# Kernel tuning notes

Measured on AMD Instinct MI355X. Metric: run time of the kernel, lower is better.

Reference implementation:

```python
import jax, jax.numpy as jnp
import numpy as np

T_STEPS = 60   # args.T
DT = 0.5       # args.dt

def rho(x):
    # repo's rho: hard-sigmoid clamp to [0, 1]
    return jnp.clip(x, 0.0, 1.0)

def setup_inputs() -> dict:
    key = jax.random.key(0)
    k1, k2, k3, k4 = jax.random.split(key, 4)
    B, n0, n1, n_in = 256, 512, 2048, 4096  # size_tab = [n0, n1, n_in]
    data = jax.random.uniform(k1, (B, n_in), dtype=jnp.float32)
    s0 = jnp.zeros((B, n0), jnp.float32)  # initHidden -> zeros
    s1 = jnp.zeros((B, n1), jnp.float32)
    # Linear-style init scales
    w0 = jax.random.normal(k2, (n0, n1), jnp.float32) / np.sqrt(n1)   # Linear(n1->n0), bias
    b0 = jnp.zeros((n0,), jnp.float32)
    w1 = jnp.transpose(w0)                                            # backward weights = w0^T (angle=0)
    w2 = jax.random.normal(k4, (n1, n_in), jnp.float32) / np.sqrt(n_in)  # Linear(n_in->n1), bias
    b2 = jnp.zeros((n1,), jnp.float32)
    return {"data": data, "s0": s0, "s1": s1, "w0": w0, "b0": b0, "w1": w1, "w2": w2, "b2": b2}

def reference(data, s0, s1, w0, b0, w1, w2, b2):
    # forward(method='nograd', beta=0): T forward-Euler stepper iterations, clamped states.
    rd = rho(data)
    inp1 = rd @ w2.T + b2  # data drive is constant over time; hoist out of the scan

    def step(carry, _):
        s0, s1 = carry
        ds0 = -s0 + rho(s1) @ w0.T + b0
        ds1 = -s1 + inp1 + rho(s0) @ w1.T
        s0 = jnp.clip(s0 + DT * ds0, 0.0, 1.0)
        s1 = jnp.clip(s1 + DT * ds1, 0.0, 1.0)
        return (s0, s1), None

    (s0, s1), _ = jax.lax.scan(step, (s0, s1), None, length=T_STEPS)
    return (s0, s1)
```

## Files before the change

### kernel.cpp

```cpp
#include <hip/hip_runtime.h>

typedef unsigned short u16;
typedef __attribute__((ext_vector_type(8))) short short8;
typedef __attribute__((ext_vector_type(4))) float f32x4;

#define BATCH 256
#define N0    512
#define N1    2048
#define NIN   4096
#define TSTEPS 60

static __device__ __forceinline__ f32x4 MFMA(short8 a, short8 b, f32x4 c) {
    return __builtin_amdgcn_mfma_f32_16x16x32_bf16(a, b, c, 0, 0, 0);
}

static __device__ __forceinline__ void split1(float x, u16* __restrict__ hp, u16* __restrict__ lp) {
    unsigned bx = __float_as_uint(x);
    *hp = (u16)(bx >> 16);
    float lf = x - __uint_as_float(bx & 0xFFFF0000u);
    *lp = (u16)(__float_as_uint(lf) >> 16);
}

static __device__ __forceinline__ float clamp01(float v) {
    return fminf(fmaxf(v, 0.0f), 1.0f);
}

static __device__ __forceinline__ size_t apos(int row, int col, int KT) {
    return ((size_t)((row >> 4) * KT + (col >> 5)) * 64
            + (size_t)((row & 15) | (((col >> 3) & 3) << 4))) * 8 + (col & 7);
}

__global__ __launch_bounds__(256) void prep_kernel(
    const float* __restrict__ w0, const float* __restrict__ w1,
    const float* __restrict__ w2, const float* __restrict__ data,
    const float* __restrict__ s0, const float* __restrict__ s1,
    u16* __restrict__ w0h, u16* __restrict__ w0l,
    u16* __restrict__ w1h, u16* __restrict__ w1l,
    u16* __restrict__ w2h, u16* __restrict__ w2l,
    u16* __restrict__ dh,  u16* __restrict__ dl,
    float* __restrict__ s0f, float* __restrict__ s1f,
    u16* __restrict__ s0h, u16* __restrict__ s0l,
    u16* __restrict__ s1h, u16* __restrict__ s1l)
{
    const int tid = blockIdx.x * 256 + threadIdx.x;
    const int nth = gridDim.x * 256;
    u16 h, l;
    for (int i = tid; i < N0 * N1; i += nth) {
        split1(w0[i], &h, &l);
        size_t p = apos(i >> 11, i & 2047, 64);
        w0h[p] = h; w0l[p] = l;
        split1(w1[i], &h, &l);
        p = apos(i >> 9, i & 511, 16);
        w1h[p] = h; w1l[p] = l;
        split1(data[i], &h, &l);
        p = apos(i >> 12, i & 4095, 128);
        dh[p] = h; dl[p] = l;
    }
    for (int i = tid; i < N1 * NIN; i += nth) {
        split1(w2[i], &h, &l);
        size_t p = apos(i >> 12, i & 4095, 128);
        w2h[p] = h; w2l[p] = l;
    }
    for (int i = tid; i < BATCH * N0; i += nth) {
        float v = s0[i]; s0f[i] = v;
        split1(v, &h, &l);
        size_t p = apos(i >> 9, i & 511, 16);
        s0h[p] = h; s0l[p] = l;
    }
    for (int i = tid; i < BATCH * N1; i += nth) {
        float v = s1[i]; s1f[i] = v;
        split1(v, &h, &l);
        size_t p = apos(i >> 11, i & 2047, 64);
        s1h[p] = h; s1l[p] = l;
    }
}

__global__ __launch_bounds__(256) void inp1_kernel(
    const u16* __restrict__ dh, const u16* __restrict__ dl,
    const u16* __restrict__ w2h, const u16* __restrict__ w2l,
    float* __restrict__ partial)
{
    const int wave = threadIdx.x >> 6, lane = threadIdx.x & 63;
    const int lrow = lane & 15, lr4 = (lane >> 4) << 2;
    const int wid = (int)blockIdx.x * 4 + wave;
    const int chunk = wid >> 11, t = wid & 2047;
    const int mt = t >> 7, nt = t & 127;
    const int kt0 = chunk * 32;

    const u16* pah = dh  + ((size_t)(mt * 128 + kt0) * 64 + lane) * 8;
    const u16* pal = dl  + ((size_t)(mt * 128 + kt0) * 64 + lane) * 8;
    const u16* pbh = w2h + ((size_t)(nt * 128 + kt0) * 64 + lane) * 8;
    const u16* pbl = w2l + ((size_t)(nt * 128 + kt0) * 64 + lane) * 8;

    f32x4 acc0 = {}, acc1 = {}, acc2 = {};
    #pragma unroll 4
    for (int i = 0; i < 32; ++i) {
        short8 ah = *(const short8*)(pah + i * 512);
        short8 al = *(const short8*)(pal + i * 512);
        short8 bh = *(const short8*)(pbh + i * 512);
        short8 bl = *(const short8*)(pbl + i * 512);
        acc0 = MFMA(ah, bh, acc0);
        acc1 = MFMA(ah, bl, acc1);
        acc2 = MFMA(al, bh, acc2);
    }
    float* out = partial + (size_t)chunk * BATCH * N1;
    const int col = nt * 16 + lrow;
    #pragma unroll
    for (int r = 0; r < 4; ++r) {
        const int row = mt * 16 + lr4 + r;
        out[(size_t)row * N1 + col] = acc0[r] + acc1[r] + acc2[r];
    }
}

__global__ __launch_bounds__(256) void reduce_kernel(
    const float* __restrict__ partial, const float* __restrict__ b2,
    float* __restrict__ inp1)
{
    const int e = blockIdx.x * 256 + threadIdx.x;
    const float4* p0 = (const float4*)partial;
    const float4* p1 = p0 + (BATCH * N1 / 4);
    const float4* p2 = p1 + (BATCH * N1 / 4);
    const float4* p3 = p2 + (BATCH * N1 / 4);
    const float4 b = ((const float4*)b2)[e & (N1 / 4 - 1)];
    float4 a0 = p0[e], a1 = p1[e], a2 = p2[e], a3 = p3[e];
    float4 r;
    r.x = a0.x + a1.x + a2.x + a3.x + b.x;
    r.y = a0.y + a1.y + a2.y + a3.y + b.y;
    r.z = a0.z + a1.z + a2.z + a3.z + b.z;
    r.w = a0.w + a1.w + a2.w + a3.w + b.w;
    ((float4*)inp1)[e] = r;
}

__global__ __launch_bounds__(256, 6) void step_kernel(
    const float* __restrict__ s0f_in, const float* __restrict__ s1f_in,
    const u16* __restrict__ s0h, const u16* __restrict__ s0l,
    const u16* __restrict__ s1h, const u16* __restrict__ s1l,
    const u16* __restrict__ w0h, const u16* __restrict__ w0l,
    const u16* __restrict__ w1h, const u16* __restrict__ w1l,
    const float* __restrict__ inp1, const float* __restrict__ b0,
    float* __restrict__ s0f_out, float* __restrict__ s1f_out,
    u16* __restrict__ s0h_out, u16* __restrict__ s0l_out,
    u16* __restrict__ s1h_out, u16* __restrict__ s1l_out)
{
    __shared__ float red[4][16][32];
    const int wg = blockIdx.x;
    const int wave = threadIdx.x >> 6, lane = threadIdx.x & 63;
    const int lrow = lane & 15, lr4 = (lane >> 4) << 2;
    const int tid = (int)threadIdx.x;

    if (wg < 1024) {
        const int mt = wg >> 6, ng = wg & 63;
        const int nfrag = wave & 1, kh = wave >> 1;
        const int nt = ng * 2 + nfrag;
        const u16* pah = s0h + ((size_t)(mt * 16 + kh * 8) * 64 + lane) * 8;
        const u16* pal = s0l + ((size_t)(mt * 16 + kh * 8) * 64 + lane) * 8;
        const u16* pbh = w1h + ((size_t)(nt * 16 + kh * 8) * 64 + lane) * 8;
        const u16* pbl = w1l + ((size_t)(nt * 16 + kh * 8) * 64 + lane) * 8;
        f32x4 acc0 = {}, acc1 = {}, acc2 = {};
        #pragma unroll 4
        for (int i = 0; i < 8; ++i) {
            short8 ah = *(const short8*)(pah + i * 512);
            short8 al = *(const short8*)(pal + i * 512);
            short8 bh = *(const short8*)(pbh + i * 512);
            short8 bl = *(const short8*)(pbl + i * 512);
            acc0 = MFMA(ah, bh, acc0);
            acc1 = MFMA(ah, bl, acc1);
            acc2 = MFMA(al, bh, acc2);
        }
        #pragma unroll
        for (int r = 0; r < 4; ++r)
            red[kh][lr4 + r][nfrag * 16 + lrow] = acc0[r] + acc1[r] + acc2[r];
        __syncthreads();
        const int mbase = mt * 16, nbase = ng * 32;
        #pragma unroll
        for (int e = tid; e < 512; e += 256) {
            const int r_ = e >> 5, c_ = e & 31;
            const int row = mbase + r_, col = nbase + c_;
            const float sum = red[0][r_][c_] + red[1][r_][c_];
            const size_t idx = (size_t)row * N1 + col;
            float v = 0.5f * (s1f_in[idx] + inp1[idx] + sum);
            v = clamp01(v);
            s1f_out[idx] = v;
            u16 h, l; split1(v, &h, &l);
            const size_t p = apos(row, col, 64);
            s1h_out[p] = h; s1l_out[p] = l;
        }
    } else {
        const int local = wg - 1024;
        const int rt = local >> 5, ct = local & 31;
        const u16* pah = s1h + ((size_t)(rt * 64 + wave * 16) * 64 + lane) * 8;
        const u16* pal = s1l + ((size_t)(rt * 64 + wave * 16) * 64 + lane) * 8;
        const u16* pbh = w0h + ((size_t)(ct * 64 + wave * 16) * 64 + lane) * 8;
        const u16* pbl = w0l + ((size_t)(ct * 64 + wave * 16) * 64 + lane) * 8;
        f32x4 acc0 = {}, acc1 = {}, acc2 = {};
        #pragma unroll 4
        for (int i = 0; i < 16; ++i) {
            short8 ah = *(const short8*)(pah + i * 512);
            short8 al = *(const short8*)(pal + i * 512);
            short8 bh = *(const short8*)(pbh + i * 512);
            short8 bl = *(const short8*)(pbl + i * 512);
            acc0 = MFMA(ah, bh, acc0);
            acc1 = MFMA(ah, bl, acc1);
            acc2 = MFMA(al, bh, acc2);
        }
        #pragma unroll
        for (int r = 0; r < 4; ++r)
            red[wave][lr4 + r][lrow] = acc0[r] + acc1[r] + acc2[r];
        __syncthreads();
        {
            const int r_ = tid >> 4, c_ = tid & 15;
            const int row = rt * 16 + r_, col = ct * 16 + c_;
            const float sum = red[0][r_][c_] + red[1][r_][c_]
                            + red[2][r_][c_] + red[3][r_][c_];
            const size_t idx = (size_t)row * N0 + col;
            float v = 0.5f * (s0f_in[idx] + sum + b0[col]);
            v = clamp01(v);
            s0f_out[idx] = v;
            u16 h, l; split1(v, &h, &l);
            const size_t p = apos(row, col, 16);
            s0h_out[p] = h; s0l_out[p] = l;
        }
    }
}

extern "C" void kernel_launch(void* const* d_in, const int* in_sizes, int n_in,
                              void* d_out, int out_size, void* d_ws, size_t ws_size,
                              hipStream_t stream) {
    const float* data = (const float*)d_in[0];
    const float* s0_0 = (const float*)d_in[1];
    const float* s1_0 = (const float*)d_in[2];
    const float* w0   = (const float*)d_in[3];
    const float* b0   = (const float*)d_in[4];
    const float* w1   = (const float*)d_in[5];
    const float* w2   = (const float*)d_in[6];
    const float* b2   = (const float*)d_in[7];

    char* p = (char*)d_ws;
    auto alloc = [&](size_t bytes) -> char* {
        char* r = p;
        p += (bytes + 255) & ~(size_t)255;
        return r;
    };
    u16* w0h = (u16*)alloc(N0 * N1 * sizeof(u16));
    u16* w0l = (u16*)alloc(N0 * N1 * sizeof(u16));
    u16* w1h = (u16*)alloc(N0 * N1 * sizeof(u16));
    u16* w1l = (u16*)alloc(N0 * N1 * sizeof(u16));
    u16* w2h = (u16*)alloc((size_t)N1 * NIN * sizeof(u16));
    u16* w2l = (u16*)alloc((size_t)N1 * NIN * sizeof(u16));
    u16* dh  = (u16*)alloc((size_t)BATCH * NIN * sizeof(u16));
    u16* dl  = (u16*)alloc((size_t)BATCH * NIN * sizeof(u16));
    float* partial = (float*)alloc((size_t)4 * BATCH * N1 * sizeof(float));
    float* inp1 = (float*)alloc((size_t)BATCH * N1 * sizeof(float));
    float* s0f[2], *s1f[2];
    u16 *s0h[2], *s0l[2], *s1h[2], *s1l[2];
    for (int i = 0; i < 2; ++i) {
        s0f[i] = (float*)alloc((size_t)BATCH * N0 * sizeof(float));
        s1f[i] = (float*)alloc((size_t)BATCH * N1 * sizeof(float));
        s0h[i] = (u16*)alloc((size_t)BATCH * N0 * sizeof(u16));
        s0l[i] = (u16*)alloc((size_t)BATCH * N0 * sizeof(u16));
        s1h[i] = (u16*)alloc((size_t)BATCH * N1 * sizeof(u16));
        s1l[i] = (u16*)alloc((size_t)BATCH * N1 * sizeof(u16));
    }

    prep_kernel<<<2048, 256, 0, stream>>>(w0, w1, w2, data, s0_0, s1_0,
                                          w0h, w0l, w1h, w1l, w2h, w2l, dh, dl,
                                          s0f[0], s1f[0], s0h[0], s0l[0], s1h[0], s1l[0]);

    inp1_kernel<<<2048, 256, 0, stream>>>(dh, dl, w2h, w2l, partial);
    reduce_kernel<<<BATCH * N1 / 4 / 256, 256, 0, stream>>>(partial, b2, inp1);

    float* out_s0 = (float*)d_out;
    float* out_s1 = (float*)d_out + (size_t)BATCH * N0;

    for (int t = 0; t < TSTEPS; ++t) {
        const int cur = t & 1, nxt = cur ^ 1;
        float* s0o = (t == TSTEPS - 1) ? out_s0 : s0f[nxt];
        float* s1o = (t == TSTEPS - 1) ? out_s1 : s1f[nxt];
        step_kernel<<<1536, 256, 0, stream>>>(
            s0f[cur], s1f[cur],
            s0h[cur], s0l[cur], s1h[cur], s1l[cur],
            w0h, w0l, w1h, w1l,
            inp1, b0,
            s0o, s1o,
            s0h[nxt], s0l[nxt], s1h[nxt], s1l[nxt]);
    }
}
```

Measured before the change: 953.5 us.

## Enlarge per-wave MFMA tiles, vectorize weight packing, and shrink step grid

The prep kernel now packs the hi/lo bf16 splits tile by tile, using vectorized float4 reads and short8 writes instead of scattered per-element stores. The inp1 and step kernels move to 512-thread blocks where each wave computes two N fragments, so each A fragment is reused across two B fragments. The s1 update no longer needs a split-K reduction through LDS, and the s0 path uses larger 32x32 tiles with a 2-way K split. The step grid falls from 1536 to 256 blocks, which cuts redundant operand loads but may leave many CUs idle and lowers parallelism.

```diff
diff --git a/kernel.cpp b/kernel.cpp
--- a/kernel.cpp
+++ b/kernel.cpp
@@ -28,6 +28,34 @@
 static __device__ __forceinline__ size_t apos(int row, int col, int KT) {
     return ((size_t)((row >> 4) * KT + (col >> 5)) * 64
             + (size_t)((row & 15) | (((col >> 3) & 3) << 4))) * 8 + (col & 7);
+}
+
+static __device__ __forceinline__ void pack_tiles(
+    const float* __restrict__ src, u16* __restrict__ dsth, u16* __restrict__ dstl,
+    int n8, int ktlog, int K, int tid, int nth)
+{
+    for (int g = tid; g < n8; g += nth) {
+        const int t = g >> 6, lane = g & 63;
+        const int rt = t >> ktlog, kt = t & ((1 << ktlog) - 1);
+        const int row = rt * 16 + (lane & 15);
+        const int col = kt * 32 + ((lane >> 4) << 3);
+        const float* s = src + (size_t)row * K + col;
+        const float4 x0 = *(const float4*)s;
+        const float4 x1 = *(const float4*)(s + 4);
+        float xs[8] = {x0.x, x0.y, x0.z, x0.w, x1.x, x1.y, x1.z, x1.w};
+        union { short8 v; unsigned u[4]; } H, L;
+        #pragma unroll
+        for (int j = 0; j < 4; ++j) {
+            unsigned ba = __float_as_uint(xs[2*j]);
+            unsigned bb = __float_as_uint(xs[2*j+1]);
+            H.u[j] = (ba >> 16) | (bb & 0xFFFF0000u);
+            float la = xs[2*j]   - __uint_as_float(ba & 0xFFFF0000u);
+            float lb = xs[2*j+1] - __uint_as_float(bb & 0xFFFF0000u);
+            L.u[j] = (__float_as_uint(la) >> 16) | (__float_as_uint(lb) & 0xFFFF0000u);
+        }
+        *(short8*)(dsth + (size_t)g * 8) = H.v;
+        *(short8*)(dstl + (size_t)g * 8) = L.v;
+    }
 }
 
 __global__ __launch_bounds__(256) void prep_kernel(
@@ -44,71 +72,66 @@
 {
     const int tid = blockIdx.x * 256 + threadIdx.x;
     const int nth = gridDim.x * 256;
-    u16 h, l;
-    for (int i = tid; i < N0 * N1; i += nth) {
-        split1(w0[i], &h, &l);
-        size_t p = apos(i >> 11, i & 2047, 64);
-        w0h[p] = h; w0l[p] = l;
-        split1(w1[i], &h, &l);
-        p = apos(i >> 9, i & 511, 16);
-        w1h[p] = h; w1l[p] = l;
-        split1(data[i], &h, &l);
-        p = apos(i >> 12, i & 4095, 128);
-        dh[p] = h; dl[p] = l;
-    }
-    for (int i = tid; i < N1 * NIN; i += nth) {
-        split1(w2[i], &h, &l);
-        size_t p = apos(i >> 12, i & 4095, 128);
-        w2h[p] = h; w2l[p] = l;
-    }
-    for (int i = tid; i < BATCH * N0; i += nth) {
-        float v = s0[i]; s0f[i] = v;
-        split1(v, &h, &l);
-        size_t p = apos(i >> 9, i & 511, 16);
-        s0h[p] = h; s0l[p] = l;
-    }
-    for (int i = tid; i < BATCH * N1; i += nth) {
-        float v = s1[i]; s1f[i] = v;
-        split1(v, &h, &l);
-        size_t p = apos(i >> 11, i & 2047, 64);
-        s1h[p] = h; s1l[p] = l;
-    }
-}
-
-__global__ __launch_bounds__(256) void inp1_kernel(
+    pack_tiles(w0,   w0h, w0l, N0 * N1 / 8,        6, N1,  tid, nth);
+    pack_tiles(w1,   w1h, w1l, N1 * N0 / 8,        4, N0,  tid, nth);
+    pack_tiles(w2,   w2h, w2l, N1 * NIN / 8,       7, NIN, tid, nth);
+    pack_tiles(data, dh,  dl,  BATCH * NIN / 8,    7, NIN, tid, nth);
+    pack_tiles(s0,   s0h, s0l, BATCH * N0 / 8,     4, N0,  tid, nth);
+    pack_tiles(s1,   s1h, s1l, BATCH * N1 / 8,     6, N1,  tid, nth);
+    for (int i = tid; i < BATCH * N0 / 4; i += nth)
+        ((float4*)s0f)[i] = ((const float4*)s0)[i];
+    for (int i = tid; i < BATCH * N1 / 4; i += nth)
+        ((float4*)s1f)[i] = ((const float4*)s1)[i];
+}
+
+__global__ __launch_bounds__(512, 2) void inp1_kernel(
     const u16* __restrict__ dh, const u16* __restrict__ dl,
     const u16* __restrict__ w2h, const u16* __restrict__ w2l,
     float* __restrict__ partial)
 {
     const int wave = threadIdx.x >> 6, lane = threadIdx.x & 63;
     const int lrow = lane & 15, lr4 = (lane >> 4) << 2;
-    const int wid = (int)blockIdx.x * 4 + wave;
-    const int chunk = wid >> 11, t = wid & 2047;
-    const int mt = t >> 7, nt = t & 127;
+    const int b = blockIdx.x;
+    const int chunk = b >> 7, rem = b & 127;
+    const int mt = rem >> 5, nt = rem & 31;
+    const int wm = wave >> 1, wn = wave & 1;
+    const int fm = mt * 4 + wm;
+    const int fn0 = nt * 4 + wn * 2;
     const int kt0 = chunk * 32;
 
-    const u16* pah = dh  + ((size_t)(mt * 128 + kt0) * 64 + lane) * 8;
-    const u16* pal = dl  + ((size_t)(mt * 128 + kt0) * 64 + lane) * 8;
-    const u16* pbh = w2h + ((size_t)(nt * 128 + kt0) * 64 + lane) * 8;
-    const u16* pbl = w2l + ((size_t)(nt * 128 + kt0) * 64 + lane) * 8;
-
-    f32x4 acc0 = {}, acc1 = {}, acc2 = {};
+    const u16* pah = dh  + ((size_t)(fm  * 128 + kt0) * 64 + lane) * 8;
+    const u16* pal = dl  + ((size_t)(fm  * 128 + kt0) * 64 + lane) * 8;
+    const u16* pb0h = w2h + ((size_t)(fn0 * 128 + kt0) * 64 + lane) * 8;
+    const u16* pb0l = w2l + ((size_t)(fn0 * 128 + kt0) * 64 + lane) * 8;
+    const u16* pb1h = pb0h + (size_t)128 * 512;
+    const u16* pb1l = pb0l + (size_t)128 * 512;
+
+    f32x4 acc[2][3] = {};
     #pragma unroll 4
     for (int i = 0; i < 32; ++i) {
-        short8 ah = *(const short8*)(pah + i * 512);
-        short8 al = *(const short8*)(pal + i * 512);
-        short8 bh = *(const short8*)(pbh + i * 512);
-        short8 bl = *(const short8*)(pbl + i * 512);
-        acc0 = MFMA(ah, bh, acc0);
-        acc1 = MFMA(ah, bl, acc1);
-        acc2 = MFMA(al, bh, acc2);
+        const int off = i * 512;
+        short8 ah = *(const short8*)(pah + off);
+        short8 al = *(const short8*)(pal + off);
+        short8 b0h_ = *(const short8*)(pb0h + off);
+        short8 b0l_ = *(const short8*)(pb0l + off);
+        short8 b1h_ = *(const short8*)(pb1h + off);
+        short8 b1l_ = *(const short8*)(pb1l + off);
+        acc[0][0] = MFMA(ah, b0h_, acc[0][0]);
+        acc[0][1] = MFMA(ah, b0l_, acc[0][1]);
+        acc[0][2] = MFMA(al, b0h_, acc[0][2]);
+        acc[1][0] = MFMA(ah, b1h_, acc[1][0]);
+        acc[1][1] = MFMA(ah, b1l_, acc[1][1]);
+        acc[1][2] = MFMA(al, b1h_, acc[1][2]);
     }
     float* out = partial + (size_t)chunk * BATCH * N1;
-    const int col = nt * 16 + lrow;
     #pragma unroll
-    for (int r = 0; r < 4; ++r) {
-        const int row = mt * 16 + lr4 + r;
-        out[(size_t)row * N1 + col] = acc0[r] + acc1[r] + acc2[r];
+    for (int n = 0; n < 2; ++n) {
+        const int col = nt * 64 + wn * 32 + n * 16 + lrow;
+        #pragma unroll
+        for (int r = 0; r < 4; ++r) {
+            const int row = mt * 64 + wm * 16 + lr4 + r;
+            out[(size_t)row * N1 + col] = acc[n][0][r] + acc[n][1][r] + acc[n][2][r];
+        }
     }
 }
 
@@ -131,7 +154,7 @@
     ((float4*)inp1)[e] = r;
 }
 
-__global__ __launch_bounds__(256, 6) void step_kernel(
+__global__ __launch_bounds__(512, 2) void step_kernel(
     const float* __restrict__ s0f_in, const float* __restrict__ s1f_in,
     const u16* __restrict__ s0h, const u16* __restrict__ s0l,
     const u16* __restrict__ s1h, const u16* __restrict__ s1l,
@@ -142,76 +165,89 @@
     u16* __restrict__ s0h_out, u16* __restrict__ s0l_out,
     u16* __restrict__ s1h_out, u16* __restrict__ s1l_out)
 {
-    __shared__ float red[4][16][32];
-    const int wg = blockIdx.x;
+    __shared__ float red[2][32][32];
+    const int b = blockIdx.x;
     const int wave = threadIdx.x >> 6, lane = threadIdx.x & 63;
     const int lrow = lane & 15, lr4 = (lane >> 4) << 2;
     const int tid = (int)threadIdx.x;
 
-    if (wg < 1024) {
-        const int mt = wg >> 6, ng = wg & 63;
-        const int nfrag = wave & 1, kh = wave >> 1;
-        const int nt = ng * 2 + nfrag;
-        const u16* pah = s0h + ((size_t)(mt * 16 + kh * 8) * 64 + lane) * 8;
-        const u16* pal = s0l + ((size_t)(mt * 16 + kh * 8) * 64 + lane) * 8;
-        const u16* pbh = w1h + ((size_t)(nt * 16 + kh * 8) * 64 + lane) * 8;
-        const u16* pbl = w1l + ((size_t)(nt * 16 + kh * 8) * 64 + lane) * 8;
+    if (b < 128) {
+        const int mt = b >> 5, ng = b & 31;
+        const int wm = wave >> 1, wn = wave & 1;
+        const int fm = mt * 4 + wm;
+        const int fn0 = ng * 4 + wn * 2;
+        const u16* pah = s0h + ((size_t)(fm * 16) * 64 + lane) * 8;
+        const u16* pal = s0l + ((size_t)(fm * 16) * 64 + lane) * 8;
+        const u16* pb0h = w1h + ((size_t)(fn0 * 16) * 64 + lane) * 8;
+        const u16* pb0l = w1l + ((size_t)(fn0 * 16) * 64 + lane) * 8;
+        const u16* pb1h = pb0h + (size_t)16 * 512;
+        const u16* pb1l = pb0l + (size_t)16 * 512;
+
+        f32x4 acc[2][3] = {};
+        #pragma unroll 4
+        for (int i = 0; i < 16; ++i) {
+            const int off = i * 512;
+            short8 ah = *(const short8*)(pah + off);
+            short8 al = *(const short8*)(pal + off);
+            short8 b0h_ = *(const short8*)(pb0h + off);
+            short8 b0l_ = *(const short8*)(pb0l + off);
+            short8 b1h_ = *(const short8*)(pb1h + off);
+            short8 b1l_ = *(const short8*)(pb1l + off);
+            acc[0][0] = MFMA(ah, b0h_, acc[0][0]);
+            acc[0][1] = MFMA(ah, b0l_, acc[0][1]);
+            acc[0][2] = MFMA(al, b0h_, acc[0][2]);
+            acc[1][0] = MFMA(ah, b1h_, acc[1][0]);
+            acc[1][1] = MFMA(ah, b1l_, acc[1][1]);
+            acc[1][2] = MFMA(al, b1h_, acc[1][2]);
+        }
+        const int mrow = mt * 64 + wm * 16;
+        #pragma unroll
+        for (int n = 0; n < 2; ++n) {
+            const int col = ng * 64 + wn * 32 + n * 16 + lrow;
+            #pragma unroll
+            for (int r = 0; r < 4; ++r) {
+                const int row = mrow + lr4 + r;
+                const size_t idx = (size_t)row * N1 + col;
+                const float sum = acc[n][0][r] + acc[n][1][r] + acc[n][2][r];
+                float v = 0.5f * (s1f_in[idx] + inp1[idx] + sum);
+                v = clamp01(v);
+                s1f_out[idx] = v;
+                u16 h, l; split1(v, &h, &l);
+                const size_t p = apos(row, col, 64);
+                s1h_out[p] = h; s1l_out[p] = l;
+            }
+        }
+    } else {
+        const int local = b - 128;
+        const int rt = local >> 4, ct = local & 15;
+        const int kh = wave >> 2, wm = (wave >> 1) & 1, wn = wave & 1;
+        const int fm = rt * 2 + wm, fn = ct * 2 + wn;
+        const u16* pah = s1h + ((size_t)(fm * 64 + kh * 32) * 64 + lane) * 8;
+        const u16* pal = s1l + ((size_t)(fm * 64 + kh * 32) * 64 + lane) * 8;
+        const u16* pbh = w0h + ((size_t)(fn * 64 + kh * 32) * 64 + lane) * 8;
+        const u16* pbl = w0l + ((size_t)(fn * 64 + kh * 32) * 64 + lane) * 8;
+
         f32x4 acc0 = {}, acc1 = {}, acc2 = {};
         #pragma unroll 4
-        for (int i = 0; i < 8; ++i) {
-            short8 ah = *(const short8*)(pah + i * 512);
-            short8 al = *(const short8*)(pal + i * 512);
-            short8 bh = *(const short8*)(pbh + i * 512);
-            short8 bl = *(const short8*)(pbl + i * 512);
+        for (int i = 0; i < 32; ++i) {
+            const int off = i * 512;
+            short8 ah = *(const short8*)(pah + off);
+            short8 al = *(const short8*)(pal + off);
+            short8 bh = *(const short8*)(pbh + off);
+            short8 bl = *(const short8*)(pbl + off);
             acc0 = MFMA(ah, bh, acc0);
             acc1 = MFMA(ah, bl, acc1);
             acc2 = MFMA(al, bh, acc2);
         }
         #pragma unroll
         for (int r = 0; r < 4; ++r)
-            red[kh][lr4 + r][nfrag * 16 + lrow] = acc0[r] + acc1[r] + acc2[r];
+            red[kh][wm * 16 + lr4 + r][wn * 16 + lrow] = acc0[r] + acc1[r] + acc2[r];
         __syncthreads();
-        const int mbase = mt * 16, nbase = ng * 32;
-        #pragma unroll
-        for (int e = tid; e < 512; e += 256) {
+        #pragma unroll
+        for (int e = tid; e < 1024; e += 512) {
             const int r_ = e >> 5, c_ = e & 31;
-            const int row = mbase + r_, col = nbase + c_;
+            const int row = rt * 32 + r_, col = ct * 32 + c_;
             const float sum = red[0][r_][c_] + red[1][r_][c_];
-            const size_t idx = (size_t)row * N1 + col;
-            float v = 0.5f * (s1f_in[idx] + inp1[idx] + sum);
-            v = clamp01(v);
-            s1f_out[idx] = v;
-            u16 h, l; split1(v, &h, &l);
-            const size_t p = apos(row, col, 64);
-            s1h_out[p] = h; s1l_out[p] = l;
-        }
-    } else {
-        const int local = wg - 1024;
-        const int rt = local >> 5, ct = local & 31;
-        const u16* pah = s1h + ((size_t)(rt * 64 + wave * 16) * 64 + lane) * 8;
-        const u16* pal = s1l + ((size_t)(rt * 64 + wave * 16) * 64 + lane) * 8;
-        const u16* pbh = w0h + ((size_t)(ct * 64 + wave * 16) * 64 + lane) * 8;
-        const u16* pbl = w0l + ((size_t)(ct * 64 + wave * 16) * 64 + lane) * 8;
-        f32x4 acc0 = {}, acc1 = {}, acc2 = {};
-        #pragma unroll 4
-        for (int i = 0; i < 16; ++i) {
-            short8 ah = *(const short8*)(pah + i * 512);
-            short8 al = *(const short8*)(pal + i * 512);
-            short8 bh = *(const short8*)(pbh + i * 512);
-            short8 bl = *(const short8*)(pbl + i * 512);
-            acc0 = MFMA(ah, bh, acc0);
-            acc1 = MFMA(ah, bl, acc1);
-            acc2 = MFMA(al, bh, acc2);
-        }
-        #pragma unroll
-        for (int r = 0; r < 4; ++r)
-            red[wave][lr4 + r][lrow] = acc0[r] + acc1[r] + acc2[r];
-        __syncthreads();
-        {
-            const int r_ = tid >> 4, c_ = tid & 15;
-            const int row = rt * 16 + r_, col = ct * 16 + c_;
-            const float sum = red[0][r_][c_] + red[1][r_][c_]
-                            + red[2][r_][c_] + red[3][r_][c_];
             const size_t idx = (size_t)row * N0 + col;
             float v = 0.5f * (s0f_in[idx] + sum + b0[col]);
             v = clamp01(v);
@@ -266,7 +302,7 @@
                                           w0h, w0l, w1h, w1l, w2h, w2l, dh, dl,
                                           s0f[0], s1f[0], s0h[0], s0l[0], s1h[0], s1l[0]);
 
-    inp1_kernel<<<2048, 256, 0, stream>>>(dh, dl, w2h, w2l, partial);
+    inp1_kernel<<<512, 512, 0, stream>>>(dh, dl, w2h, w2l, partial);
     reduce_kernel<<<BATCH * N1 / 4 / 256, 256, 0, stream>>>(partial, b2, inp1);
 
     float* out_s0 = (float*)d_out;
@@ -276,7 +312,7 @@
         const int cur = t & 1, nxt = cur ^ 1;
         float* s0o = (t == TSTEPS - 1) ? out_s0 : s0f[nxt];
         float* s1o = (t == TSTEPS - 1) ? out_s1 : s1f[nxt];
-        step_kernel<<<1536, 256, 0, stream>>>(
+        step_kernel<<<256, 512, 0, stream>>>(
             s0f[cur], s1f[cur],
             s0h[cur], s0l[cur], s1h[cur], s1l[cur],
             w0h, w0l, w1h, w1l,
```

Measured after the change: 978.5 us. 1.03x slower.
